# Kernel optimization log

Measured on AMD Instinct MI355X. Metric: run time of the kernel, lower is better.

## Reference

```python
import jax, jax.numpy as jnp
import numpy as np

T, G, D = 64, 1024, 128      # timesteps, detections per timestep, feature dim
N = T * G                    # total points; output rows = 3 + D = 131 cols


def setup_inputs() -> dict:
    key = jax.random.key(0)
    k1, k2 = jax.random.split(key)
    # time column: T distinct timestamps, G detections each (already time-sorted)
    times = jnp.repeat(jnp.arange(T, dtype=jnp.float32), G)
    xy = jax.random.uniform(k1, (N, 2), dtype=jnp.float32) * 128.0
    coor = jnp.concatenate([times[:, None], xy], axis=1)          # [N, 3]
    features = jax.random.normal(k2, (N, D), dtype=jnp.float32)   # [N, 128]
    return {"coor": coor, "features": features, "min_length": 8}


def _traverse(nxt):
    """Greedy chain building with a visited set (faithful to the torch loop).
    nxt[i] = precomputed best cosine match of point i in the next time group
    (-1 if i is in the last group). Returns (out_nodes, cid, clen):
      out_nodes[p] = node emitted at output slot p (all N slots filled),
      cid[p]       = chain id of slot p,
      clen[c]      = length of chain c.
    """
    def chain_cond(carry):
        visited, out, cid, p, cur, length, c = carry
        nx = nxt[cur]
        return (nx >= 0) & (~visited[nx])

    def chain_body(carry):
        visited, out, cid, p, cur, length, c = carry
        nx = nxt[cur]
        visited = visited.at[nx].set(True)
        out = out.at[p].set(nx)
        cid = cid.at[p].set(c)
        return (visited, out, cid, p + 1, nx, length + 1, c)

    def start_chain(st, start):
        visited, out, cid, clen, p, c = st
        visited = visited.at[start].set(True)
        out = out.at[p].set(start)
        cid = cid.at[p].set(c)
        carry = (visited, out, cid, p + 1, start, jnp.int32(1), c)
        visited, out, cid, p, cur, length, _ = jax.lax.while_loop(
            chain_cond, chain_body, carry)
        clen = clen.at[c].set(length)
        return (visited, out, cid, clen, p, c + 1)

    def body(start, st):
        start = jnp.int32(start)
        return jax.lax.cond(st[0][start], lambda s: s,
                            lambda s: start_chain(s, start), st)

    init = (jnp.zeros(N, bool),
            jnp.full(N, -1, jnp.int32),
            jnp.zeros(N, jnp.int32),
            jnp.zeros(N, jnp.int32),
            jnp.int32(0), jnp.int32(0))
    visited, out, cid, clen, p, c = jax.lax.fori_loop(0, N, body, init)
    return out, cid, clen


def reference(coor, features, min_length):
    # sort all points by time (stable; input is already time-sorted)
    order = jnp.argsort(coor[:, 0], stable=True)
    coor = coor[order]
    features = features[order]

    # --- vectorized precompute of the greedy next-match graph ---
    # group points by timestamp: [T, G, D]
    f = features.reshape(T, G, D)
    fn = f / jnp.maximum(jnp.linalg.norm(f, axis=-1, keepdims=True), 1e-6)
    # cosine sims between each time group and the next one: [T-1, G, G]
    sims = jnp.einsum('tgd,thd->tgh', fn[:-1], fn[1:])
    best = jnp.argmax(sims, axis=-1).astype(jnp.int32)        # [T-1, G]
    nxt = jnp.concatenate([
        (jnp.arange(1, T, dtype=jnp.int32)[:, None] * G + best).reshape(-1),
        jnp.full((G,), -1, jnp.int32)])                        # [N]
    nxt = jax.lax.stop_gradient(nxt)

    # --- sequential greedy traversal with visited set ---
    out_nodes, cid, clen = _traverse(nxt)

    # rows = [coor || features] in trajectory order
    rows = jnp.concatenate([coor, features], axis=1)[out_nodes]  # [N, 3+D]
    keep = clen[cid] >= min_length
    # pack kept rows to the top (order preserved), zero-pad the rest
    perm = jnp.argsort(~keep, stable=True)
    return jnp.where(keep[perm][:, None], rows[perm], 0.0)       # [N, 131]
```

## Files before the change

kernel.cpp:

```cpp
#include <hip/hip_runtime.h>
#include <hip/hip_bf16.h>
#include <hip/hip_fp16.h>

#define TT 64
#define GN 1024
#define DK 128
#define NN (TT * GN)
#define OUTC 131
#define TAU 5e-3f
#define CHUNK 64

typedef _Float16 f16x8 __attribute__((ext_vector_type(8)));
typedef float    f32x4 __attribute__((ext_vector_type(4)));

__device__ __forceinline__ unsigned f2h(float f) {
    return (unsigned)__half_as_ushort(__float2half(f));
}

__device__ __forceinline__ void gload_lds16(const void* g, void* l) {
    __builtin_amdgcn_global_load_lds(
        (const __attribute__((address_space(1))) unsigned int*)g,
        (__attribute__((address_space(3))) unsigned int*)l, 16, 0, 0);
}

__global__ void kconv(const float* __restrict__ feat, unsigned* __restrict__ fh,
                      float* __restrict__ rnf, double* __restrict__ rnd,
                      int* __restrict__ rcnt, int* __restrict__ clen) {
    if (blockIdx.x == 0 && threadIdx.x < 63) rcnt[threadIdx.x] = 0;
    if (blockIdx.x < 256) clen[blockIdx.x * 256 + threadIdx.x] = 0;
    int row  = blockIdx.x * 4 + (threadIdx.x >> 6);
    int lane = threadIdx.x & 63;
    const float* fr = feat + (size_t)row * DK;
    float2 v = *(const float2*)(fr + lane * 2);
    fh[(size_t)row * 64 + lane] = f2h(v.x) | (f2h(v.y) << 16);
    double s = (double)v.x * (double)v.x + (double)v.y * (double)v.y;
    #pragma unroll
    for (int off = 32; off > 0; off >>= 1)
        s += __shfl_down(s, off);
    if (lane == 0) {
        double m = sqrt(s);
        if (m < 1e-6) m = 1e-6;
        double r = 1.0 / m;
        rnd[row] = r;
        rnf[row] = (float)r;
    }
}

__global__ __launch_bounds__(256) void ksim(const unsigned* __restrict__ fh,
                                            const float* __restrict__ rnf,
                                            float4* __restrict__ tws) {
    __shared__ int Atile[8192];
    __shared__ int Btile[8192];

    int id = blockIdx.x;
    int t  = id >> 6;
    int mt = (id >> 3) & 7;
    int nt = id & 7;

    int tid  = threadIdx.x;
    int wave = tid >> 6;
    int lane = tid & 63;
    int la = lane & 15;
    int lq = lane >> 4;
    int wr = (wave & 1) * 64;
    int wc = (wave >> 1) * 64;

    const int* Ag = (const int*)fh + ((size_t)t * GN + mt * 128) * 64;
    const int* Bg = (const int*)fh + ((size_t)(t + 1) * GN + nt * 128) * 64;

    #pragma unroll
    for (int i = 0; i < 8; ++i) {
        int L = i * 256 + tid;
        int row = L >> 4, colL = L & 15;
        int colG = colL ^ (row & 7);
        gload_lds16(Ag + row * 64 + colG * 4, &Atile[L * 4]);
        gload_lds16(Bg + row * 64 + colG * 4, &Btile[L * 4]);
    }
    __syncthreads();

    f32x4 acc[4][4];
    #pragma unroll
    for (int at = 0; at < 4; ++at)
        #pragma unroll
        for (int ct = 0; ct < 4; ++ct) acc[at][ct] = (f32x4){0.f, 0.f, 0.f, 0.f};

    #pragma unroll
    for (int kc = 0; kc < 4; ++kc) {
        int sw = ((kc * 4 + lq) ^ (la & 7)) << 2;
        f16x8 af[4], bf[4];
        #pragma unroll
        for (int x = 0; x < 4; ++x) {
            af[x] = __builtin_bit_cast(f16x8, *(const int4*)&Atile[(wr + x * 16 + la) * 64 + sw]);
            bf[x] = __builtin_bit_cast(f16x8, *(const int4*)&Btile[(wc + x * 16 + la) * 64 + sw]);
        }
        #pragma unroll
        for (int at = 0; at < 4; ++at)
            #pragma unroll
            for (int ct = 0; ct < 4; ++ct)
                acc[at][ct] = __builtin_amdgcn_mfma_f32_16x16x32_f16(
                    bf[ct], af[at], acc[at][ct], 0, 0, 0);
    }

    float t1[4], t2[4]; int i1[4];
    #pragma unroll
    for (int s = 0; s < 4; ++s) { t1[s] = -3.4e38f; t2[s] = -3.4e38f; i1[s] = 0x7fffffff; }

    const float* rB = rnf + (size_t)(t + 1) * GN + nt * 128;
    #pragma unroll
    for (int ct = 0; ct < 4; ++ct) {
        float4 rnv = *(const float4*)&rB[wc + ct * 16 + lq * 4];
        int nbase = nt * 128 + wc + ct * 16 + lq * 4;
        float rn[4] = {rnv.x, rnv.y, rnv.z, rnv.w};
        #pragma unroll
        for (int at = 0; at < 4; ++at) {
            #pragma unroll
            for (int reg = 0; reg < 4; ++reg) {
                float v = acc[at][ct][reg] * rn[reg];
                t2[at] = fmaxf(t2[at], fminf(v, t1[at]));
                if (v > t1[at]) { t1[at] = v; i1[at] = nbase + reg; }
            }
        }
    }

    #pragma unroll
    for (int m = 16; m <= 32; m <<= 1) {
        #pragma unroll
        for (int s = 0; s < 4; ++s) {
            float o1 = __shfl_xor(t1[s], m);
            float o2 = __shfl_xor(t2[s], m);
            int   oi = __shfl_xor(i1[s], m);
            bool take = (o1 > t1[s]) || (o1 == t1[s] && oi < i1[s]);
            float nt2 = take ? fmaxf(o2, t1[s]) : fmaxf(t2[s], o1);
            if (take) { t1[s] = o1; i1[s] = oi; }
            t2[s] = nt2;
        }
    }

    __syncthreads();
    float* mv1 = (float*)Atile;
    float* mv2 = mv1 + 256;
    int*   mi1 = (int*)(mv2 + 256);
    if (lq == 0) {
        #pragma unroll
        for (int s = 0; s < 4; ++s) {
            int row = wr + s * 16 + la;
            int idx = row * 2 + (wave >> 1);
            mv1[idx] = t1[s]; mv2[idx] = t2[s]; mi1[idx] = i1[s];
        }
    }
    __syncthreads();

    if (tid < 128) {
        float best = mv1[tid * 2], sec, bw2 = mv2[tid * 2];
        int bi = mi1[tid * 2];
        float v1 = mv1[tid * 2 + 1], v2 = mv2[tid * 2 + 1];
        int  ii = mi1[tid * 2 + 1];
        if (v1 > best || (v1 == best && ii < bi)) {
            sec = fmaxf(best, v2); best = v1; bi = ii;
        } else {
            sec = fmaxf(v1, bw2);
        }
        float4 o; o.x = best; o.y = sec; o.z = __int_as_float(bi); o.w = 0.f;
        tws[((size_t)(nt * 63 + t)) * GN + mt * 128 + tid] = o;
    }
}

__global__ void kmerge(const float4* __restrict__ tws, unsigned short* __restrict__ nxt16,
                       int* __restrict__ rcnt, int* __restrict__ rlistT) {
    int idx = blockIdx.x * 256 + threadIdx.x;
    int t = idx >> 10, grow = idx & 1023;
    float best = -3.4e38f, sec = -3.4e38f, bw2 = -3.4e38f;
    int bi = 0x7fffffff;
    #pragma unroll
    for (int nb = 0; nb < 8; ++nb) {
        float4 v = tws[((size_t)(nb * 63 + t)) * GN + grow];
        int ii = __float_as_int(v.z);
        if (v.x > best || (v.x == best && ii < bi)) {
            sec = fmaxf(sec, best);
            best = v.x; bi = ii; bw2 = v.y;
        } else {
            sec = fmaxf(sec, v.x);
        }
    }
    sec = fmaxf(sec, bw2);
    if (best - sec < TAU) {
        int p = atomicAdd(&rcnt[t], 1);
        rlistT[t * 1024 + p] = grow;
    } else {
        nxt16[idx] = (unsigned short)bi;
    }
}

#define ACC4(sv, aa, bb)                                   \
    sv = fma((double)(aa).x, (double)(bb).x, sv);          \
    sv = fma((double)(aa).y, (double)(bb).y, sv);          \
    sv = fma((double)(aa).z, (double)(bb).z, sv);          \
    sv = fma((double)(aa).w, (double)(bb).w, sv);

__global__ __launch_bounds__(256) void krescue(const float* __restrict__ feat,
                                               const double* __restrict__ rnd,
                                               const int* __restrict__ rcnt,
                                               const int* __restrict__ rlistT,
                                               double* __restrict__ pbv,
                                               int* __restrict__ pbi) {
    __shared__ float  arows[CHUNK][128];
    __shared__ int    rl[CHUNK];
    __shared__ double cv[4][128];
    __shared__ int    ci[4][128];
    __shared__ double resv[CHUNK];
    __shared__ int    resi[CHUNK];
    int bid = blockIdx.x;
    int t = bid >> 2, q = bid & 3;
    int nr = rcnt[t];
    if (nr == 0) return;
    int tid  = threadIdx.x;
    int wave = tid >> 6, lane = tid & 63;
    int row  = tid >> 1;
    int par  = tid & 1;
    int h0 = q * 256 + row;
    int h1 = h0 + 128;

    const float* B0 = feat + ((size_t)(t + 1) * GN + h0) * DK + par * 64;
    const float* B1 = feat + ((size_t)(t + 1) * GN + h1) * DK + par * 64;
    float4 br0[16], br1[16];
    #pragma unroll
    for (int i = 0; i < 16; ++i) {
        br0[i] = *(const float4*)(B0 + i * 4);
        br1[i] = *(const float4*)(B1 + i * 4);
    }
    double rb0 = rnd[(t + 1) * GN + h0];
    double rb1 = rnd[(t + 1) * GN + h1];

    for (int c0 = 0; c0 < nr; c0 += CHUNK) {
        int cn = min(CHUNK, nr - c0);
        if (tid < cn) rl[tid] = rlistT[t * 1024 + c0 + tid];
        __syncthreads();
        for (int e = tid; e < cn * 32; e += 256) {
            int r = e >> 5, k = e & 31;
            *(float4*)&arows[r][k * 4] =
                *(const float4*)(feat + ((size_t)t * GN + rl[r]) * DK + k * 4);
        }
        __syncthreads();

        for (int rb = 0; rb < cn; rb += 4) {
            int rn4 = min(4, cn - rb);
            for (int rr = 0; rr < rn4; ++rr) {
                const float* ap = &arows[rb + rr][par * 64];
                double s0=0.0,s1=0.0,s2=0.0,s3=0.0;
                double u0=0.0,u1=0.0,u2=0.0,u3=0.0;
                #pragma unroll
                for (int i = 0; i < 16; i += 4) {
                    float4 a0 = *(const float4*)(ap + i * 4);
                    float4 a1 = *(const float4*)(ap + i * 4 + 4);
                    float4 a2 = *(const float4*)(ap + i * 4 + 8);
                    float4 a3 = *(const float4*)(ap + i * 4 + 12);
                    ACC4(s0, a0, br0[i])     ACC4(s1, a1, br0[i + 1])
                    ACC4(s2, a2, br0[i + 2]) ACC4(s3, a3, br0[i + 3])
                    ACC4(u0, a0, br1[i])     ACC4(u1, a1, br1[i + 1])
                    ACC4(u2, a2, br1[i + 2]) ACC4(u3, a3, br1[i + 3])
                }
                double s = (s0 + s1) + (s2 + s3);
                double u = (u0 + u1) + (u2 + u3);
                double so = __shfl_xor(s, 1);
                double uo = __shfl_xor(u, 1);
                if (par == 0) {
                    double v0 = (s + so) * rb0;
                    double v1 = (u + uo) * rb1;
                    if (v1 > v0) { cv[rr][row] = v1; ci[rr][row] = h1; }
                    else         { cv[rr][row] = v0; ci[rr][row] = h0; }
                }
            }
            __syncthreads();
            if (wave < rn4) {
                double v1 = cv[wave][lane];      int i1 = ci[wave][lane];
                double v2 = cv[wave][lane + 64]; int i2 = ci[wave][lane + 64];
                if (v2 > v1 || (v2 == v1 && i2 < i1)) { v1 = v2; i1 = i2; }
                #pragma unroll
                for (int off = 32; off > 0; off >>= 1) {
                    double ov = __shfl_down(v1, off);
                    int    oi = __shfl_down(i1, off);
                    if (ov > v1 || (ov == v1 && oi < i1)) { v1 = ov; i1 = oi; }
                }
                if (lane == 0) { resv[rb + wave] = v1; resi[rb + wave] = i1; }
            }
            __syncthreads();
        }

        if (tid < cn) {
            pbv[(size_t)bid * 1024 + c0 + tid] = resv[tid];
            pbi[(size_t)bid * 1024 + c0 + tid] = resi[tid];
        }
        __syncthreads();
    }
}

__global__ __launch_bounds__(1024) void kgraph(const unsigned short* __restrict__ nxt16,
                                               const int* __restrict__ rcnt,
                                               const int* __restrict__ rlistT,
                                               const double* __restrict__ pbv,
                                               const int* __restrict__ pbi,
                                               int* __restrict__ chain_of) {
    __shared__ unsigned short ns[64 * 1024];
    __shared__ int winner[2 * GN];
    __shared__ int rc[64];
    int g = threadIdx.x;

    #pragma unroll
    for (int i = 0; i < 8; ++i)
        gload_lds16((const char*)nxt16 + ((size_t)i * 1024 + g) * 16,
                    (char*)ns + ((size_t)i * 1024 + g) * 16);

    if (g < 63) rc[g] = rcnt[g];
    winner[g] = 0x7fffffff;
    chain_of[g] = g;
    __syncthreads();

    int t0 = g >> 4;
    if (t0 < TT - 1) {
        for (int ri = g & 15; ri < rc[t0]; ri += 16) {
            double bv = -1e300; int bi = 0x7fffffff;
            #pragma unroll
            for (int q = 0; q < 4; ++q) {
                double v  = pbv[(size_t)(t0 * 4 + q) * 1024 + ri];
                int    ii = pbi[(size_t)(t0 * 4 + q) * 1024 + ri];
                if (v > bv || (v == bv && ii < bi)) { bv = v; bi = ii; }
            }
            ns[t0 * GN + rlistT[t0 * 1024 + ri]] = (unsigned short)bi;
        }
    }
    __syncthreads();

    int mychain = g;
    for (int t = 0; t < TT - 1; ++t) {
        int* Wa = winner + (t & 1) * GN;
        int* Wb = winner + ((t + 1) & 1) * GN;
        int j = ns[t * GN + g];
        atomicMin(&Wa[j], mychain);
        Wb[g] = 0x7fffffff;
        __syncthreads();
        int w = Wa[g];
        mychain = (w == 0x7fffffff) ? (((t + 1) << 10) | g) : w;
        ns[t * GN + g] = (unsigned short)mychain;
        __syncthreads();
    }

    for (int t = 0; t < TT - 1; ++t)
        chain_of[(t + 1) * GN + g] = ns[t * GN + g];
}

__global__ void kclen(const int* __restrict__ chain_of, int* __restrict__ clen) {
    int i = blockIdx.x * 256 + threadIdx.x;
    atomicAdd(&clen[chain_of[i]], 1);
}

__global__ __launch_bounds__(1024) void kseg(const int* __restrict__ chain_of,
                                             const int* __restrict__ clen,
                                             const int* __restrict__ minp,
                                             int* __restrict__ oloc,
                                             int* __restrict__ partial) {
    __shared__ int ps[1024];
    int b = blockIdx.x, tid = threadIdx.x;
    int i = b * 1024 + tid;
    int ml = *minp;
    int cl = clen[i];
    int v = (chain_of[i] == i && cl >= ml) ? cl : 0;
    ps[tid] = v;
    __syncthreads();
    for (int off = 1; off < 1024; off <<= 1) {
        int add = (tid >= off) ? ps[tid - off] : 0;
        __syncthreads();
        ps[tid] += add;
        __syncthreads();
    }
    oloc[i] = ps[tid] - v;
    if (tid == 1023) partial[b] = ps[tid];
}

__global__ __launch_bounds__(256) void kout(const float* __restrict__ coor,
                                            const float* __restrict__ feat,
                                            const int* __restrict__ chain_of,
                                            const int* __restrict__ clen,
                                            const int* __restrict__ oloc,
                                            const int* __restrict__ partial,
                                            const int* __restrict__ minp,
                                            float* __restrict__ out) {
    __shared__ int pb[64];
    __shared__ int stot;
    int tid = threadIdx.x;
    if (tid < 64) {
        int v = partial[tid];
        int acc = v;
        #pragma unroll
        for (int off = 1; off < 64; off <<= 1) {
            int o = __shfl_up(acc, off);
            if (tid >= off) acc += o;
        }
        pb[tid] = acc - v;
        if (tid == 63) stot = acc;
    }
    __syncthreads();

    int node = blockIdx.x * 4 + (tid >> 6);
    int lane = tid & 63;
    int s = chain_of[node];
    if (clen[s] >= *minp) {
        int row = oloc[s] + pb[s >> 10] + (node >> 10) - (s >> 10);
        float* orow = out + (size_t)row * OUTC;
        const float* f = feat + (size_t)node * DK;
        if (lane < 3) orow[lane] = coor[(size_t)node * 3 + lane];
        orow[3 + lane]  = f[lane];
        orow[67 + lane] = f[64 + lane];
    }

    int zrow = stot + blockIdx.x * 4 + (tid >> 6);
    if (zrow < NN) {
        float* orow = out + (size_t)zrow * OUTC;
        orow[lane] = 0.f;
        orow[64 + lane] = 0.f;
        if (lane < 3) orow[128 + lane] = 0.f;
    }
}

extern "C" void kernel_launch(void* const* d_in, const int* in_sizes, int n_in,
                              void* d_out, int out_size, void* d_ws, size_t ws_size,
                              hipStream_t stream) {
    const float* coor   = (const float*)d_in[0];
    const float* feat   = (const float*)d_in[1];
    const int*   minlen = (const int*)d_in[2];
    float*       out    = (float*)d_out;

    char* ws = (char*)d_ws;
    double*         rnd      = (double*)(ws);
    float*          rnf      = (float*)(ws + 524288);
    unsigned short* nxt16    = (unsigned short*)(ws + 786432);
    int*            chain_of = (int*)(ws + 917504);
    int*            clen     = (int*)(ws + 1179648);
    int*            oloc     = (int*)(ws + 1441792);
    int*            rcnt     = (int*)(ws + 1703936);
    int*            partial  = (int*)(ws + 1704192);
    int*            rlistT   = (int*)(ws + 1705216);
    unsigned*       fh       = (unsigned*)(ws + 2097152);
    float4*         tws      = (float4*)(ws + 18874368);
    double*         pbv      = (double*)(ws + 18874368);
    int*            pbi      = (int*)(ws + 18874368 + 2064384);

    kconv<<<NN / 4, 256, 0, stream>>>(feat, fh, rnf, rnd, rcnt, clen);

    ksim<<<63 * 64, 256, 0, stream>>>(fh, rnf, tws);

    kmerge<<<63 * GN / 256, 256, 0, stream>>>(tws, nxt16, rcnt, rlistT);
    krescue<<<63 * 4, 256, 0, stream>>>(feat, rnd, rcnt, rlistT, pbv, pbi);

    kgraph<<<1, GN, 0, stream>>>(nxt16, rcnt, rlistT, pbv, pbi, chain_of);
    kclen<<<NN / 256, 256, 0, stream>>>(chain_of, clen);
    kseg<<<64, 1024, 0, stream>>>(chain_of, clen, minlen, oloc, partial);
    kout<<<NN / 4, 256, 0, stream>>>(coor, feat, chain_of, clen, oloc, partial,
                                     minlen, out);
}
```

Before: 232.2 us.

## Fuse argmax merge into similarity kernel with double-buffered B tiles

Each ksim block now keeps its 128-row A tile resident in registers and loops over all eight 128-column B tiles of the next timestep. The next B tile is prefetched into a double-buffered LDS slot while the current one is multiplied. The block keeps a running top-1/top-2 per row and writes nxt16 or the rescue list directly, which removes the separate kmerge kernel and the float4 intermediate buffer round-trip. The cost is 8x fewer blocks (504 instead of 4032), so less parallelism across CUs, plus more registers for the held A fragments and a sync per B tile.

```diff
diff --git a/kernel.cpp b/kernel.cpp
--- a/kernel.cpp
+++ b/kernel.cpp
@@ -48,14 +48,14 @@
 
 __global__ __launch_bounds__(256) void ksim(const unsigned* __restrict__ fh,
                                             const float* __restrict__ rnf,
-                                            float4* __restrict__ tws) {
-    __shared__ int Atile[8192];
-    __shared__ int Btile[8192];
+                                            unsigned short* __restrict__ nxt16,
+                                            int* __restrict__ rcnt,
+                                            int* __restrict__ rlistT) {
+    __shared__ int Tiles[3][8192];
 
     int id = blockIdx.x;
-    int t  = id >> 6;
-    int mt = (id >> 3) & 7;
-    int nt = id & 7;
+    int t  = id >> 3;
+    int mt = id & 7;
 
     int tid  = threadIdx.x;
     int wave = tid >> 6;
@@ -66,60 +66,85 @@
     int wc = (wave >> 1) * 64;
 
     const int* Ag = (const int*)fh + ((size_t)t * GN + mt * 128) * 64;
-    const int* Bg = (const int*)fh + ((size_t)(t + 1) * GN + nt * 128) * 64;
+    const int* Bg = (const int*)fh + (size_t)(t + 1) * GN * 64;
 
     #pragma unroll
     for (int i = 0; i < 8; ++i) {
         int L = i * 256 + tid;
-        int row = L >> 4, colL = L & 15;
-        int colG = colL ^ (row & 7);
-        gload_lds16(Ag + row * 64 + colG * 4, &Atile[L * 4]);
-        gload_lds16(Bg + row * 64 + colG * 4, &Btile[L * 4]);
-    }
-    __syncthreads();
-
-    f32x4 acc[4][4];
-    #pragma unroll
-    for (int at = 0; at < 4; ++at)
-        #pragma unroll
-        for (int ct = 0; ct < 4; ++ct) acc[at][ct] = (f32x4){0.f, 0.f, 0.f, 0.f};
-
+        int row = L >> 4, colG = (L & 15) ^ (row & 7);
+        gload_lds16(Ag + row * 64 + colG * 4, &Tiles[2][L * 4]);
+        gload_lds16(Bg + row * 64 + colG * 4, &Tiles[0][L * 4]);
+    }
+    __syncthreads();
+
+    f16x8 af[4][4];
     #pragma unroll
     for (int kc = 0; kc < 4; ++kc) {
         int sw = ((kc * 4 + lq) ^ (la & 7)) << 2;
-        f16x8 af[4], bf[4];
-        #pragma unroll
-        for (int x = 0; x < 4; ++x) {
-            af[x] = __builtin_bit_cast(f16x8, *(const int4*)&Atile[(wr + x * 16 + la) * 64 + sw]);
-            bf[x] = __builtin_bit_cast(f16x8, *(const int4*)&Btile[(wc + x * 16 + la) * 64 + sw]);
-        }
+        #pragma unroll
+        for (int x = 0; x < 4; ++x)
+            af[kc][x] = __builtin_bit_cast(f16x8,
+                *(const int4*)&Tiles[2][(wr + x * 16 + la) * 64 + sw]);
+    }
+
+    float t1[4], t2[4]; int i1[4];
+    #pragma unroll
+    for (int s = 0; s < 4; ++s) { t1[s] = -3.4e38f; t2[s] = -3.4e38f; i1[s] = 0x7fffffff; }
+
+    const float* rB = rnf + (size_t)(t + 1) * GN;
+
+    #pragma unroll 2
+    for (int ntb = 0; ntb < 8; ++ntb) {
+        int cur = ntb & 1;
+        if (ntb < 7) {
+            const int* Bn = Bg + (ntb + 1) * 128 * 64;
+            int* dst = Tiles[cur ^ 1];
+            #pragma unroll
+            for (int i = 0; i < 8; ++i) {
+                int L = i * 256 + tid;
+                int row = L >> 4, colG = (L & 15) ^ (row & 7);
+                gload_lds16(Bn + row * 64 + colG * 4, &dst[L * 4]);
+            }
+        }
+
+        f32x4 acc[4][4];
         #pragma unroll
         for (int at = 0; at < 4; ++at)
             #pragma unroll
-            for (int ct = 0; ct < 4; ++ct)
-                acc[at][ct] = __builtin_amdgcn_mfma_f32_16x16x32_f16(
-                    bf[ct], af[at], acc[at][ct], 0, 0, 0);
-    }
-
-    float t1[4], t2[4]; int i1[4];
-    #pragma unroll
-    for (int s = 0; s < 4; ++s) { t1[s] = -3.4e38f; t2[s] = -3.4e38f; i1[s] = 0x7fffffff; }
-
-    const float* rB = rnf + (size_t)(t + 1) * GN + nt * 128;
-    #pragma unroll
-    for (int ct = 0; ct < 4; ++ct) {
-        float4 rnv = *(const float4*)&rB[wc + ct * 16 + lq * 4];
-        int nbase = nt * 128 + wc + ct * 16 + lq * 4;
-        float rn[4] = {rnv.x, rnv.y, rnv.z, rnv.w};
-        #pragma unroll
-        for (int at = 0; at < 4; ++at) {
-            #pragma unroll
-            for (int reg = 0; reg < 4; ++reg) {
-                float v = acc[at][ct][reg] * rn[reg];
-                t2[at] = fmaxf(t2[at], fminf(v, t1[at]));
-                if (v > t1[at]) { t1[at] = v; i1[at] = nbase + reg; }
+            for (int ct = 0; ct < 4; ++ct) acc[at][ct] = (f32x4){0.f, 0.f, 0.f, 0.f};
+
+        const int* Bt = Tiles[cur];
+        #pragma unroll
+        for (int kc = 0; kc < 4; ++kc) {
+            int sw = ((kc * 4 + lq) ^ (la & 7)) << 2;
+            f16x8 bf[4];
+            #pragma unroll
+            for (int x = 0; x < 4; ++x)
+                bf[x] = __builtin_bit_cast(f16x8, *(const int4*)&Bt[(wc + x * 16 + la) * 64 + sw]);
+            #pragma unroll
+            for (int at = 0; at < 4; ++at)
+                #pragma unroll
+                for (int ct = 0; ct < 4; ++ct)
+                    acc[at][ct] = __builtin_amdgcn_mfma_f32_16x16x32_f16(
+                        bf[ct], af[kc][at], acc[at][ct], 0, 0, 0);
+        }
+
+        #pragma unroll
+        for (int ct = 0; ct < 4; ++ct) {
+            float4 rnv = *(const float4*)&rB[ntb * 128 + wc + ct * 16 + lq * 4];
+            int nbase = ntb * 128 + wc + ct * 16 + lq * 4;
+            float rn[4] = {rnv.x, rnv.y, rnv.z, rnv.w};
+            #pragma unroll
+            for (int at = 0; at < 4; ++at) {
+                #pragma unroll
+                for (int reg = 0; reg < 4; ++reg) {
+                    float v = acc[at][ct][reg] * rn[reg];
+                    t2[at] = fmaxf(t2[at], fminf(v, t1[at]));
+                    if (v > t1[at]) { t1[at] = v; i1[at] = nbase + reg; }
+                }
             }
         }
+        __syncthreads();
     }
 
     #pragma unroll
@@ -136,8 +161,7 @@
         }
     }
 
-    __syncthreads();
-    float* mv1 = (float*)Atile;
+    float* mv1 = (float*)Tiles[2];
     float* mv2 = mv1 + 256;
     int*   mi1 = (int*)(mv2 + 256);
     if (lq == 0) {
@@ -160,34 +184,13 @@
         } else {
             sec = fmaxf(v1, bw2);
         }
-        float4 o; o.x = best; o.y = sec; o.z = __int_as_float(bi); o.w = 0.f;
-        tws[((size_t)(nt * 63 + t)) * GN + mt * 128 + tid] = o;
-    }
-}
-
-__global__ void kmerge(const float4* __restrict__ tws, unsigned short* __restrict__ nxt16,
-                       int* __restrict__ rcnt, int* __restrict__ rlistT) {
-    int idx = blockIdx.x * 256 + threadIdx.x;
-    int t = idx >> 10, grow = idx & 1023;
-    float best = -3.4e38f, sec = -3.4e38f, bw2 = -3.4e38f;
-    int bi = 0x7fffffff;
-    #pragma unroll
-    for (int nb = 0; nb < 8; ++nb) {
-        float4 v = tws[((size_t)(nb * 63 + t)) * GN + grow];
-        int ii = __float_as_int(v.z);
-        if (v.x > best || (v.x == best && ii < bi)) {
-            sec = fmaxf(sec, best);
-            best = v.x; bi = ii; bw2 = v.y;
+        int grow = mt * 128 + tid;
+        if (best - sec < TAU) {
+            int p = atomicAdd(&rcnt[t], 1);
+            rlistT[t * 1024 + p] = grow;
         } else {
-            sec = fmaxf(sec, v.x);
-        }
-    }
-    sec = fmaxf(sec, bw2);
-    if (best - sec < TAU) {
-        int p = atomicAdd(&rcnt[t], 1);
-        rlistT[t * 1024 + p] = grow;
-    } else {
-        nxt16[idx] = (unsigned short)bi;
+            nxt16[t * GN + grow] = (unsigned short)bi;
+        }
     }
 }
 
@@ -440,15 +443,13 @@
     int*            partial  = (int*)(ws + 1704192);
     int*            rlistT   = (int*)(ws + 1705216);
     unsigned*       fh       = (unsigned*)(ws + 2097152);
-    float4*         tws      = (float4*)(ws + 18874368);
     double*         pbv      = (double*)(ws + 18874368);
     int*            pbi      = (int*)(ws + 18874368 + 2064384);
 
     kconv<<<NN / 4, 256, 0, stream>>>(feat, fh, rnf, rnd, rcnt, clen);
 
-    ksim<<<63 * 64, 256, 0, stream>>>(fh, rnf, tws);
-
-    kmerge<<<63 * GN / 256, 256, 0, stream>>>(tws, nxt16, rcnt, rlistT);
+    ksim<<<63 * 8, 256, 0, stream>>>(fh, rnf, nxt16, rcnt, rlistT);
+
     krescue<<<63 * 4, 256, 0, stream>>>(feat, rnd, rcnt, rlistT, pbv, pbi);
 
     kgraph<<<1, GN, 0, stream>>>(nxt16, rcnt, rlistT, pbv, pbi, chain_of);
```

Result: faster. 227.6 us (-2.0%).
